# Kernel tuning notes

Measured on AMD Instinct MI355X. Metric: run time of the kernel, lower is better.

## Reference

```python
import jax, jax.numpy as jnp
import numpy as np

D = 64          # dim1 = dim2 = dim3
B = 512         # batch
MMHID = 256
F = (D + 1) ** 3  # 274625, encoder1 input size
SKIP = 3 * (D + 1)  # 195


def _lin(x, w, b):
    # torch nn.Linear: y = x @ W^T + b, W: [out, in]
    return x @ w.T + b


def _bilinear(x1, x2, w, b):
    # torch nn.Bilinear: y_o = x1_i W_{oij} x2_j + b_o
    return jnp.einsum('bi,oij,bj->bo', x1, w, x2) + b


def setup_inputs() -> dict:
    key = jax.random.key(0)
    ks = jax.random.split(key, 16)

    def n(k, shape, scale):
        return (jax.random.normal(k, shape, dtype=jnp.float32) * scale)

    inp = {
        'vec1': n(ks[0], (B, D), 1.0),
        'vec2': n(ks[1], (B, D), 1.0),
        'vec3': n(ks[2], (B, D), 1.0),
        # gated branch 1
        'h1_w': n(ks[3], (D, D), 1.0 / np.sqrt(D)), 'h1_b': jnp.zeros((D,), jnp.float32),
        'z1_w': n(ks[4], (D, D, D), 1.0 / D), 'z1_b': jnp.zeros((D,), jnp.float32),
        'o1_w': n(ks[5], (D, D), 1.0 / np.sqrt(D)), 'o1_b': jnp.zeros((D,), jnp.float32),
        # gated branch 2
        'h2_w': n(ks[6], (D, D), 1.0 / np.sqrt(D)), 'h2_b': jnp.zeros((D,), jnp.float32),
        'z2_w': n(ks[7], (D, D, D), 1.0 / D), 'z2_b': jnp.zeros((D,), jnp.float32),
        'o2_w': n(ks[8], (D, D), 1.0 / np.sqrt(D)), 'o2_b': jnp.zeros((D,), jnp.float32),
        # gated branch 3
        'h3_w': n(ks[9], (D, D), 1.0 / np.sqrt(D)), 'h3_b': jnp.zeros((D,), jnp.float32),
        'z3_w': n(ks[10], (D, D, D), 1.0 / D), 'z3_b': jnp.zeros((D,), jnp.float32),
        'o3_w': n(ks[11], (D, D), 1.0 / np.sqrt(D)), 'o3_b': jnp.zeros((D,), jnp.float32),
        # encoders
        'enc1_w': n(ks[12], (MMHID, F), 1.0 / np.sqrt(F)), 'enc1_b': jnp.zeros((MMHID,), jnp.float32),
        'enc2_w': n(ks[13], (MMHID, MMHID + SKIP), 1.0 / np.sqrt(MMHID + SKIP)), 'enc2_b': jnp.zeros((MMHID,), jnp.float32),
    }
    return inp


def reference(vec1, vec2, vec3,
              h1_w, h1_b, z1_w, z1_b, o1_w, o1_b,
              h2_w, h2_b, z2_w, z2_b, o2_w, o2_b,
              h3_w, h3_b, z3_w, z3_b, o3_w, o3_b,
              enc1_w, enc1_b, enc2_w, enc2_b):
    # dropout layers are identity in eval mode
    h1 = jax.nn.relu(_lin(vec1, h1_w, h1_b))
    z1 = _bilinear(vec1, vec3, z1_w, z1_b)
    o1 = jax.nn.relu(_lin(jax.nn.sigmoid(z1) * h1, o1_w, o1_b))

    h2 = jax.nn.relu(_lin(vec2, h2_w, h2_b))
    z2 = _bilinear(vec2, vec3, z2_w, z2_b)
    o2 = jax.nn.relu(_lin(jax.nn.sigmoid(z2) * h2, o2_w, o2_b))

    h3 = jax.nn.relu(_lin(vec3, h3_w, h3_b))
    z3 = _bilinear(vec1, vec3, z3_w, z3_b)  # note: z3 uses (vec1, vec3) per source
    o3 = jax.nn.relu(_lin(jax.nn.sigmoid(z3) * h3, o3_w, o3_b))

    ones = jnp.ones((o1.shape[0], 1), o1.dtype)
    o1 = jnp.concatenate([o1, ones], axis=1)  # [B, D+1]
    o2 = jnp.concatenate([o2, ones], axis=1)
    o3 = jnp.concatenate([o3, ones], axis=1)

    # trilinear outer product, flattened in (i, j, k) order matching
    # bmm(o1, o2).flatten then bmm(., o3).flatten in torch
    o123 = jnp.einsum('bi,bj,bk->bijk', o1, o2, o3).reshape(o1.shape[0], -1)  # [B, F]

    out = jax.nn.relu(_lin(o123, enc1_w, enc1_b))
    out = jnp.concatenate([out, o1, o2, o3], axis=1)  # skip connection
    out = jax.nn.relu(_lin(out, enc2_w, enc2_b))
    return out
```

## Files before the change

kernel.cpp:

```cpp
#include <hip/hip_runtime.h>
#include <hip/hip_bf16.h>
#include <stdint.h>

typedef unsigned short u16;
typedef unsigned int u32;

#define F1 274625
#define IJ1 4225

typedef float v4f __attribute__((ext_vector_type(4)));
typedef __bf16 v8bf __attribute__((ext_vector_type(8)));

__device__ __forceinline__ float lof(u32 u) { union { u32 u; float f; } c; c.u = u << 16; return c.f; }
__device__ __forceinline__ float hif(u32 u) { union { u32 u; float f; } c; c.u = u & 0xffff0000u; return c.f; }
__device__ __forceinline__ u16 f2bf(float f) {
  union { float f; u32 u; } c; c.f = f;
  u32 r = (c.u >> 16) & 1u;
  return (u16)((c.u + 0x7fffu + r) >> 16);
}
__device__ __forceinline__ u32 pkbf(u32 a, u32 b) {
  union { float f; u32 u; } ca, cb; ca.u = a; cb.u = b;
  __hip_bfloat162 h = __float22bfloat162_rn(make_float2(ca.f, cb.f));
  union { __hip_bfloat162 h; u32 u; } c; c.h = h; return c.u;
}

__global__ void __launch_bounds__(256) k0_transpose(const float* __restrict__ v1,
    const float* __restrict__ v2, const float* __restrict__ v3, float* __restrict__ xT) {
  int g = blockIdx.x * 256 + threadIdx.x;
  if (g >= 3 * 64 * 512) return;
  int t = g >> 15, r = g & 32767;
  int d = r >> 9, b = r & 511;
  const float* v = (t == 0) ? v1 : ((t == 1) ? v2 : v3);
  xT[g] = v[b * 64 + d];
}

__global__ void __launch_bounds__(256) k1_bilinear(
    const float* __restrict__ zw1, const float* __restrict__ zw2, const float* __restrict__ zw3,
    const float* __restrict__ xT, float* __restrict__ zsum) {
  int bid = blockIdx.x;
  int ih = bid & 1, bh = (bid >> 1) & 1;
  int o = (bid >> 2) & 63, t = bid >> 8;
  int b = bh * 256 + threadIdx.x;
  const float* zw = (t == 0) ? zw1 : ((t == 1) ? zw2 : zw3);
  const float* xiT = xT + ((t == 1) ? 32768 : 0);
  const float* x3T = xT + 65536;
  float x3r[64];
#pragma unroll
  for (int j = 0; j < 64; ++j) x3r[j] = x3T[j * 512 + b];
  const float4* w4 = (const float4*)(zw + o * 4096);
  float acc = 0.f;
  int i0 = ih * 32;
#pragma unroll 2
  for (int i = i0; i < i0 + 32; ++i) {
    float xi = xiT[i * 512 + b];
    float s = 0.f;
#pragma unroll
    for (int q = 0; q < 16; ++q) {
      float4 w = w4[i * 16 + q];
      s += w.x * x3r[q*4+0] + w.y * x3r[q*4+1] + w.z * x3r[q*4+2] + w.w * x3r[q*4+3];
    }
    acc += xi * s;
  }
  atomicAdd(&zsum[t * 32768 + o * 512 + b], acc);
}

__global__ void __launch_bounds__(256) k2_branch(
    const float* __restrict__ hw1, const float* __restrict__ hb1,
    const float* __restrict__ ow1, const float* __restrict__ ob1,
    const float* __restrict__ hw2, const float* __restrict__ hb2,
    const float* __restrict__ ow2, const float* __restrict__ ob2,
    const float* __restrict__ hw3, const float* __restrict__ hb3,
    const float* __restrict__ ow3, const float* __restrict__ ob3,
    const float* __restrict__ zb1, const float* __restrict__ zb2, const float* __restrict__ zb3,
    const float* __restrict__ xT, const float* __restrict__ zsum,
    float* __restrict__ oT, u16* __restrict__ o3row) {
  int t = blockIdx.x >> 3, bc = blockIdx.x & 7;
  int lane = threadIdx.x & 63;
  int w = __builtin_amdgcn_readfirstlane((int)(threadIdx.x >> 6));
  int b = bc * 64 + lane;
  const float* hw = (t==0)?hw1:((t==1)?hw2:hw3);
  const float* hb = (t==0)?hb1:((t==1)?hb2:hb3);
  const float* ow = (t==0)?ow1:((t==1)?ow2:ow3);
  const float* ob = (t==0)?ob1:((t==1)?ob2:ob3);
  const float* zb = (t==0)?zb1:((t==1)?zb2:zb3);
  const float* xtT = xT + t * 32768;
  const float4* hw4 = (const float4*)hw;
  const float4* ow4 = (const float4*)ow;
  __shared__ float gT[64][68];
  float xr[64];
#pragma unroll
  for (int k = 0; k < 64; ++k) xr[k] = xtT[k * 512 + b];
#pragma unroll
  for (int ii = 0; ii < 16; ii += 4) {
    float gv[4];
#pragma unroll
    for (int q = 0; q < 4; ++q) {
      int i = w * 16 + ii + q;
      float a = hb[i];
#pragma unroll
      for (int kq = 0; kq < 16; ++kq) {
        float4 h4 = hw4[i * 16 + kq];
        a += h4.x * xr[kq*4+0] + h4.y * xr[kq*4+1] + h4.z * xr[kq*4+2] + h4.w * xr[kq*4+3];
      }
      float hv = fmaxf(a, 0.f);
      float z = zsum[t * 32768 + i * 512 + b] + zb[i];
      float sg = 1.f / (1.f + __expf(-z));
      gv[q] = sg * hv;
    }
    *(float4*)&gT[lane][w * 16 + ii] = make_float4(gv[0], gv[1], gv[2], gv[3]);
  }
  __syncthreads();
  float gr[64];
#pragma unroll
  for (int k = 0; k < 64; k += 4) {
    float4 g4 = *(const float4*)&gT[lane][k];
    gr[k] = g4.x; gr[k+1] = g4.y; gr[k+2] = g4.z; gr[k+3] = g4.w;
  }
#pragma unroll
  for (int ii = 0; ii < 16; ++ii) {
    int oo = w * 16 + ii;
    float a = ob[oo];
#pragma unroll
    for (int kq = 0; kq < 16; ++kq) {
      float4 o4 = ow4[oo * 16 + kq];
      a += o4.x * gr[kq*4+0] + o4.y * gr[kq*4+1] + o4.z * gr[kq*4+2] + o4.w * gr[kq*4+3];
    }
    float ov = fmaxf(a, 0.f);
    oT[(t * 65 + oo) * 512 + b] = ov;
    if (t == 2) o3row[b * 72 + oo] = f2bf(ov);
  }
  if (w == 0) oT[(t * 65 + 64) * 512 + b] = 1.f;
  if (t == 2 && w == 1) {
    uint4 ones = make_uint4(0x3F80u, 0u, 0u, 0u);
    *(uint4*)&o3row[b * 72 + 64] = ones;
  }
}

template<int S4>
__device__ __forceinline__ void pack_row(const uint4* qv, char* bsB, int sxor, int hh) {
  u32 l[36];
#pragma unroll
  for (int r = 0; r < 9; ++r) {
    l[4*r+0] = qv[r].x; l[4*r+1] = qv[r].y; l[4*r+2] = qv[r].z; l[4*r+3] = qv[r].w;
  }
#pragma unroll
  for (int m = 0; m < 4; ++m) {
    u32 p0 = pkbf(l[S4+8*m+0], l[S4+8*m+1]);
    u32 p1 = pkbf(l[S4+8*m+2], l[S4+8*m+3]);
    u32 p2 = pkbf(l[S4+8*m+4], l[S4+8*m+5]);
    u32 p3 = pkbf(l[S4+8*m+6], l[S4+8*m+7]);
    *(uint4*)(bsB + ((hh*64 + m*16) ^ sxor)) = make_uint4(p0, p1, p2, p3);
  }
  if (hh) *(u16*)(bsB + 128) = (u16)(pkbf(l[S4+32], l[S4+32]) & 0xffffu);
}

__global__ void __launch_bounds__(256, 2) k4_gemm(
    const float* __restrict__ W, const u16* __restrict__ o3row,
    const float* __restrict__ oT, float* __restrict__ accum,
    float* __restrict__ pbuf, int mode) {
  __shared__ u16 o3r[128 * 72];
  __shared__ u16 Bs[128 * 72];
  __shared__ float o12sf[128];
  int bid = blockIdx.x;
  int xcd = bid & 7, slot = bid >> 3;
  int mb = slot & 3, ph = slot >> 2;
  int pair = ph * 8 + xcd;
  int sK = pair >> 1, nb = pair & 1;
  int mbase = mb * 128, nbase = nb * 128;
  int ij0 = (sK * IJ1) >> 6, ij1 = ((sK + 1) * IJ1) >> 6;
  int tid = threadIdx.x;

  for (int u = tid; u < 1024; u += 256) {
    int r = u >> 3, c = u & 7;
    const uint4 v = *(const uint4*)(o3row + (mbase + r) * 72 + c * 8);
    *(uint4*)((char*)o3r + r * 144 + ((c * 16) ^ (((r >> 2) & 7) << 4))) = v;
  }

  int lane = tid & 63;
  int wid = __builtin_amdgcn_readfirstlane(tid >> 6);
  int wm = wid >> 1, wn = wid & 1;
  int lrow = lane & 15, lkg = lane >> 4;
  int rpos = lane >> 1, hh = lane & 1;

  int aoffB[4][2], boffB[4][2], vvoff[4];
#pragma unroll
  for (int u = 0; u < 4; ++u) {
    int ra = wm * 64 + u * 16 + lrow;
    int rb = wn * 64 + u * 16 + lrow;
#pragma unroll
    for (int k2 = 0; k2 < 2; ++k2) {
      aoffB[u][k2] = ra * 144 + ((lkg * 16 + k2 * 64) ^ (((ra >> 2) & 7) << 4));
      boffB[u][k2] = rb * 144 + ((lkg * 16 + k2 * 64) ^ (((rb >> 2) & 7) << 4));
    }
    vvoff[u] = rb * 72 + 64;
  }

  v4f acc[16] = {};
  const uint4* Wq = (const uint4*)W;
  uint4 qv[9];
  float cA = 0.f, cB = 0.f;
  {
    int cc = (wid - ij0) & 3;
    int row = rpos * 4 + cc;
    long g = (long)(nbase + row) * F1 + (long)ij0 * 65;
    long u4 = (g >> 2) + (long)hh * 8;
#pragma unroll
    for (int r = 0; r < 9; ++r) qv[r] = Wq[u4 + r];
    int i = ij0 / 65, j = ij0 - i * 65;
    if (tid < 128) {
      cA = oT[i * 512 + mbase + tid];
      cB = oT[(65 + j) * 512 + mbase + tid];
    }
  }
  __syncthreads();

#pragma unroll 1
  for (int ij = ij0; ij < ij1; ++ij) {
    {
      int cc = (wid - ij) & 3;
      int row = rpos * 4 + cc;
      char* bsB = (char*)Bs + row * 144;
      int sxor = ((row >> 2) & 7) << 4;
      if      (wid == 0) pack_row<0>(qv, bsB, sxor, hh);
      else if (wid == 1) pack_row<1>(qv, bsB, sxor, hh);
      else if (wid == 2) pack_row<2>(qv, bsB, sxor, hh);
      else               pack_row<3>(qv, bsB, sxor, hh);
    }
    if (tid < 128) o12sf[tid] = cA * cB;
    if (ij + 1 < ij1) {
      int cc = (wid - (ij + 1)) & 3;
      int row = rpos * 4 + cc;
      long g = (long)(nbase + row) * F1 + (long)(ij + 1) * 65;
      long u4 = (g >> 2) + (long)hh * 8;
#pragma unroll
      for (int r = 0; r < 9; ++r) qv[r] = Wq[u4 + r];
      int i = (ij + 1) / 65, j = (ij + 1) - i * 65;
      if (tid < 128) {
        cA = oT[i * 512 + mbase + tid];
        cB = oT[(65 + j) * 512 + mbase + tid];
      }
    }
    __syncthreads();

    v8bf bf0[2], bf1[2], bf2[2], bf3[2];
#pragma unroll
    for (int k2 = 0; k2 < 2; ++k2) {
      bf0[k2] = *(const v8bf*)((const char*)Bs + boffB[0][k2]);
      bf1[k2] = *(const v8bf*)((const char*)Bs + boffB[1][k2]);
      bf2[k2] = *(const v8bf*)((const char*)Bs + boffB[2][k2]);
      bf3[k2] = *(const v8bf*)((const char*)Bs + boffB[3][k2]);
    }
    float vv0 = lof((u32)Bs[vvoff[0]]);
    float vv1 = lof((u32)Bs[vvoff[1]]);
    float vv2 = lof((u32)Bs[vvoff[2]]);
    float vv3 = lof((u32)Bs[vvoff[3]]);
#pragma unroll
    for (int t2 = 0; t2 < 4; ++t2) {
      v8bf a0 = *(const v8bf*)((const char*)o3r + aoffB[t2][0]);
      v8bf a1 = *(const v8bf*)((const char*)o3r + aoffB[t2][1]);
      v4f P0 = {}, P1 = {}, P2 = {}, P3 = {};
      P0 = __builtin_amdgcn_mfma_f32_16x16x32_bf16(a0, bf0[0], P0, 0, 0, 0);
      P0 = __builtin_amdgcn_mfma_f32_16x16x32_bf16(a1, bf0[1], P0, 0, 0, 0);
      P1 = __builtin_amdgcn_mfma_f32_16x16x32_bf16(a0, bf1[0], P1, 0, 0, 0);
      P1 = __builtin_amdgcn_mfma_f32_16x16x32_bf16(a1, bf1[1], P1, 0, 0, 0);
      P2 = __builtin_amdgcn_mfma_f32_16x16x32_bf16(a0, bf2[0], P2, 0, 0, 0);
      P2 = __builtin_amdgcn_mfma_f32_16x16x32_bf16(a1, bf2[1], P2, 0, 0, 0);
      P3 = __builtin_amdgcn_mfma_f32_16x16x32_bf16(a0, bf3[0], P3, 0, 0, 0);
      P3 = __builtin_amdgcn_mfma_f32_16x16x32_bf16(a1, bf3[1], P3, 0, 0, 0);
      float4 sp = *(const float4*)&o12sf[wm * 64 + t2 * 16 + lkg * 4];
#pragma unroll
      for (int e = 0; e < 4; ++e) {
        float se = (e == 0) ? sp.x : (e == 1) ? sp.y : (e == 2) ? sp.z : sp.w;
        acc[t2 * 4 + 0][e] += se * (P0[e] + vv0);
        acc[t2 * 4 + 1][e] += se * (P1[e] + vv1);
        acc[t2 * 4 + 2][e] += se * (P2[e] + vv2);
        acc[t2 * 4 + 3][e] += se * (P3[e] + vv3);
      }
    }
    __syncthreads();
  }

  if (mode) {
    float* dst = pbuf + ((long)sK << 17);
#pragma unroll
    for (int t2 = 0; t2 < 4; ++t2) {
      int gb0 = mbase + wm * 64 + t2 * 16 + lkg * 4;
#pragma unroll
      for (int u2 = 0; u2 < 4; ++u2) {
        int go = nbase + wn * 64 + u2 * 16 + lrow;
#pragma unroll
        for (int e = 0; e < 4; ++e)
          dst[(gb0 + e) * 256 + go] = acc[t2 * 4 + u2][e];
      }
    }
  } else {
#pragma unroll
    for (int t2 = 0; t2 < 4; ++t2) {
      int gb0 = mbase + wm * 64 + t2 * 16 + lkg * 4;
#pragma unroll
      for (int u2 = 0; u2 < 4; ++u2) {
        int go = nbase + wn * 64 + u2 * 16 + lrow;
#pragma unroll
        for (int e = 0; e < 4; ++e)
          atomicAdd(&accum[(gb0 + e) * 256 + go], acc[t2 * 4 + u2][e]);
      }
    }
  }
}

__global__ void __launch_bounds__(256) k4_reduce(const float* __restrict__ P,
                                                 float* __restrict__ accum) {
  int g = blockIdx.x * 256 + threadIdx.x;
  const v4f* p4 = (const v4f*)P;
  v4f s = p4[g];
#pragma unroll 4
  for (int k = 1; k < 64; ++k) s += p4[(k << 15) + g];
  ((v4f*)accum)[g] = s;
}

__global__ void __launch_bounds__(256) k5_enc2(
    const float* __restrict__ accum, const float* __restrict__ oT,
    const float* __restrict__ enc1b, const float* __restrict__ w2,
    const float* __restrict__ enc2b, float* __restrict__ outp) {
  int bg = blockIdx.x >> 3, og = blockIdx.x & 7;
  int lane = threadIdx.x & 63;
  int w = __builtin_amdgcn_readfirstlane((int)(threadIdx.x >> 6));
  int b = bg * 64 + lane;
  int obase = og * 32 + w * 8;
  float a8[8];
#pragma unroll
  for (int q = 0; q < 8; ++q) a8[q] = enc2b[obase + q];
  for (int c = 0; c < 256; ++c) {
    float x = fmaxf(accum[b * 256 + c] + enc1b[c], 0.f);
#pragma unroll
    for (int q = 0; q < 8; ++q) a8[q] += w2[(obase + q) * 451 + c] * x;
  }
  for (int e = 0; e < 195; ++e) {
    float x = oT[e * 512 + b];
#pragma unroll
    for (int q = 0; q < 8; ++q) a8[q] += w2[(obase + q) * 451 + 256 + e] * x;
  }
#pragma unroll
  for (int q = 0; q < 8; ++q) outp[b * 256 + obase + q] = fmaxf(a8[q], 0.f);
}

extern "C" void kernel_launch(void* const* d_in, const int* in_sizes, int n_in,
                              void* d_out, int out_size, void* d_ws, size_t ws_size,
                              hipStream_t stream) {
  const float* vec1 = (const float*)d_in[0];
  const float* vec2 = (const float*)d_in[1];
  const float* vec3 = (const float*)d_in[2];
  const float* h1w = (const float*)d_in[3];  const float* h1b = (const float*)d_in[4];
  const float* z1w = (const float*)d_in[5];  const float* z1b = (const float*)d_in[6];
  const float* o1w = (const float*)d_in[7];  const float* o1b = (const float*)d_in[8];
  const float* h2w = (const float*)d_in[9];  const float* h2b = (const float*)d_in[10];
  const float* z2w = (const float*)d_in[11]; const float* z2b = (const float*)d_in[12];
  const float* o2w = (const float*)d_in[13]; const float* o2b = (const float*)d_in[14];
  const float* h3w = (const float*)d_in[15]; const float* h3b = (const float*)d_in[16];
  const float* z3w = (const float*)d_in[17]; const float* z3b = (const float*)d_in[18];
  const float* o3w = (const float*)d_in[19]; const float* o3b = (const float*)d_in[20];
  const float* e1w = (const float*)d_in[21]; const float* e1b = (const float*)d_in[22];
  const float* e2w = (const float*)d_in[23]; const float* e2b = (const float*)d_in[24];

  char* ws = (char*)d_ws;
  float* accum = (float*)(ws + 0);
  float* oT    = (float*)(ws + 524288);
  u16* o3row   = (u16*)  (ws + 923648);
  float* xT    = (float*)(ws + 997376);
  float* zsum  = (float*)(ws + 1390592);
  float* pbuf  = (float*)(ws + 1783808);
  size_t need = 1783808 + (size_t)64 * 512 * 256 * 4;
  int mode = (ws_size >= need) ? 1 : 0;
  float* pArg = mode ? pbuf : accum;

  hipMemsetAsync(accum, 0, 524288, stream);
  hipMemsetAsync(zsum, 0, 393216, stream);

  hipLaunchKernelGGL(k0_transpose, dim3(384), dim3(256), 0, stream, vec1, vec2, vec3, xT);
  hipLaunchKernelGGL(k1_bilinear, dim3(768), dim3(256), 0, stream, z1w, z2w, z3w, xT, zsum);
  hipLaunchKernelGGL(k2_branch, dim3(24), dim3(256), 0, stream,
                     h1w, h1b, o1w, o1b, h2w, h2b, o2w, o2b, h3w, h3b, o3w, o3b,
                     z1b, z2b, z3b, xT, zsum, oT, o3row);
  hipLaunchKernelGGL(k4_gemm, dim3(512), dim3(256), 0, stream, e1w, o3row, oT, accum,
                     pArg, mode);
  if (mode)
    hipLaunchKernelGGL(k4_reduce, dim3(128), dim3(256), 0, stream, pbuf, accum);
  hipLaunchKernelGGL(k5_enc2, dim3(64), dim3(256), 0, stream, accum, oT, e1b, e2w, e2b,
                     (float*)d_out);
}
```

Measured before the change: 720.7 us.

## Double-buffer enc1 GEMM tiles, shrink M tile, drop transpose and memsets

The enc1 GEMM now uses 64-row M tiles with 1024 blocks and three blocks per CU. It double-buffers the packed bf16 weight tile in shared memory, so packing the next ij step overlaps with the MFMAs, and it raises wave priority around the MFMA section. The separate transpose kernel is removed: the bilinear and branch kernels read vec rows directly with float4 loads. The bilinear kernel covers the full i range per block and writes directly instead of using atomics, so the memsets are dropped. The reduce kernel now applies bias and ReLU and writes a transposed layout for enc2. The cost is that the XOR swizzle is removed from shared memory, which can bring back bank conflicts, and each weight tile is reused across a smaller M tile.

```diff
diff --git a/kernel.cpp b/kernel.cpp
--- a/kernel.cpp
+++ b/kernel.cpp
@@ -12,7 +12,6 @@
 typedef __bf16 v8bf __attribute__((ext_vector_type(8)));
 
 __device__ __forceinline__ float lof(u32 u) { union { u32 u; float f; } c; c.u = u << 16; return c.f; }
-__device__ __forceinline__ float hif(u32 u) { union { u32 u; float f; } c; c.u = u & 0xffff0000u; return c.f; }
 __device__ __forceinline__ u16 f2bf(float f) {
   union { float f; u32 u; } c; c.f = f;
   u32 r = (c.u >> 16) & 1u;
@@ -24,35 +23,28 @@
   union { __hip_bfloat162 h; u32 u; } c; c.h = h; return c.u;
 }
 
-__global__ void __launch_bounds__(256) k0_transpose(const float* __restrict__ v1,
-    const float* __restrict__ v2, const float* __restrict__ v3, float* __restrict__ xT) {
-  int g = blockIdx.x * 256 + threadIdx.x;
-  if (g >= 3 * 64 * 512) return;
-  int t = g >> 15, r = g & 32767;
-  int d = r >> 9, b = r & 511;
-  const float* v = (t == 0) ? v1 : ((t == 1) ? v2 : v3);
-  xT[g] = v[b * 64 + d];
-}
-
 __global__ void __launch_bounds__(256) k1_bilinear(
+    const float* __restrict__ v1, const float* __restrict__ v2, const float* __restrict__ v3,
     const float* __restrict__ zw1, const float* __restrict__ zw2, const float* __restrict__ zw3,
-    const float* __restrict__ xT, float* __restrict__ zsum) {
+    float* __restrict__ zsum) {
   int bid = blockIdx.x;
-  int ih = bid & 1, bh = (bid >> 1) & 1;
-  int o = (bid >> 2) & 63, t = bid >> 8;
+  int bh = bid & 1, o = (bid >> 1) & 63, t = bid >> 7;
   int b = bh * 256 + threadIdx.x;
   const float* zw = (t == 0) ? zw1 : ((t == 1) ? zw2 : zw3);
-  const float* xiT = xT + ((t == 1) ? 32768 : 0);
-  const float* x3T = xT + 65536;
+  const float* xv = (t == 1) ? v2 : v1;
   float x3r[64];
-#pragma unroll
-  for (int j = 0; j < 64; ++j) x3r[j] = x3T[j * 512 + b];
+  const float4* x34 = (const float4*)(v3 + b * 64);
+#pragma unroll
+  for (int q = 0; q < 16; ++q) {
+    float4 a = x34[q];
+    x3r[q*4+0] = a.x; x3r[q*4+1] = a.y; x3r[q*4+2] = a.z; x3r[q*4+3] = a.w;
+  }
   const float4* w4 = (const float4*)(zw + o * 4096);
+  const float* xrow = xv + b * 64;
   float acc = 0.f;
-  int i0 = ih * 32;
-#pragma unroll 2
-  for (int i = i0; i < i0 + 32; ++i) {
-    float xi = xiT[i * 512 + b];
+#pragma unroll 4
+  for (int i = 0; i < 64; ++i) {
+    float xi = xrow[i];
     float s = 0.f;
 #pragma unroll
     for (int q = 0; q < 16; ++q) {
@@ -61,10 +53,11 @@
     }
     acc += xi * s;
   }
-  atomicAdd(&zsum[t * 32768 + o * 512 + b], acc);
+  zsum[t * 32768 + o * 512 + b] = acc;
 }
 
 __global__ void __launch_bounds__(256) k2_branch(
+    const float* __restrict__ v1, const float* __restrict__ v2, const float* __restrict__ v3,
     const float* __restrict__ hw1, const float* __restrict__ hb1,
     const float* __restrict__ ow1, const float* __restrict__ ob1,
     const float* __restrict__ hw2, const float* __restrict__ hb2,
@@ -72,7 +65,7 @@
     const float* __restrict__ hw3, const float* __restrict__ hb3,
     const float* __restrict__ ow3, const float* __restrict__ ob3,
     const float* __restrict__ zb1, const float* __restrict__ zb2, const float* __restrict__ zb3,
-    const float* __restrict__ xT, const float* __restrict__ zsum,
+    const float* __restrict__ zsum,
     float* __restrict__ oT, u16* __restrict__ o3row) {
   int t = blockIdx.x >> 3, bc = blockIdx.x & 7;
   int lane = threadIdx.x & 63;
@@ -83,13 +76,17 @@
   const float* ow = (t==0)?ow1:((t==1)?ow2:ow3);
   const float* ob = (t==0)?ob1:((t==1)?ob2:ob3);
   const float* zb = (t==0)?zb1:((t==1)?zb2:zb3);
-  const float* xtT = xT + t * 32768;
+  const float* xv = (t==0)?v1:((t==1)?v2:v3);
   const float4* hw4 = (const float4*)hw;
   const float4* ow4 = (const float4*)ow;
   __shared__ float gT[64][68];
   float xr[64];
-#pragma unroll
-  for (int k = 0; k < 64; ++k) xr[k] = xtT[k * 512 + b];
+  const float4* xv4 = (const float4*)(xv + b * 64);
+#pragma unroll
+  for (int q = 0; q < 16; ++q) {
+    float4 a = xv4[q];
+    xr[q*4+0] = a.x; xr[q*4+1] = a.y; xr[q*4+2] = a.z; xr[q*4+3] = a.w;
+  }
 #pragma unroll
   for (int ii = 0; ii < 16; ii += 4) {
     float gv[4];
@@ -137,7 +134,7 @@
 }
 
 template<int S4>
-__device__ __forceinline__ void pack_row(const uint4* qv, char* bsB, int sxor, int hh) {
+__device__ __forceinline__ void pack_row(const uint4* qv, u16* bp, int hh) {
   u32 l[36];
 #pragma unroll
   for (int r = 0; r < 9; ++r) {
@@ -149,179 +146,154 @@
     u32 p1 = pkbf(l[S4+8*m+2], l[S4+8*m+3]);
     u32 p2 = pkbf(l[S4+8*m+4], l[S4+8*m+5]);
     u32 p3 = pkbf(l[S4+8*m+6], l[S4+8*m+7]);
-    *(uint4*)(bsB + ((hh*64 + m*16) ^ sxor)) = make_uint4(p0, p1, p2, p3);
-  }
-  if (hh) *(u16*)(bsB + 128) = (u16)(pkbf(l[S4+32], l[S4+32]) & 0xffffu);
-}
-
-__global__ void __launch_bounds__(256, 2) k4_gemm(
+    *(uint4*)(bp + hh * 32 + m * 8) = make_uint4(p0, p1, p2, p3);
+  }
+  if (hh) bp[64] = (u16)(pkbf(l[S4+32], l[S4+32]) & 0xffffu);
+}
+
+__global__ void __launch_bounds__(256, 3) k4_gemm(
     const float* __restrict__ W, const u16* __restrict__ o3row,
     const float* __restrict__ oT, float* __restrict__ accum,
     float* __restrict__ pbuf, int mode) {
-  __shared__ u16 o3r[128 * 72];
-  __shared__ u16 Bs[128 * 72];
-  __shared__ float o12sf[128];
+  __shared__ u16 o3r[64 * 72];
+  __shared__ u16 Bs[2][128 * 72];
+  __shared__ float o12sf[2][64];
   int bid = blockIdx.x;
   int xcd = bid & 7, slot = bid >> 3;
-  int mb = slot & 3, ph = slot >> 2;
+  int mb = slot & 7, ph = slot >> 3;
   int pair = ph * 8 + xcd;
   int sK = pair >> 1, nb = pair & 1;
-  int mbase = mb * 128, nbase = nb * 128;
+  int mbase = mb * 64, nbase = nb * 128;
   int ij0 = (sK * IJ1) >> 6, ij1 = ((sK + 1) * IJ1) >> 6;
   int tid = threadIdx.x;
-
-  for (int u = tid; u < 1024; u += 256) {
-    int r = u >> 3, c = u & 7;
-    const uint4 v = *(const uint4*)(o3row + (mbase + r) * 72 + c * 8);
-    *(uint4*)((char*)o3r + r * 144 + ((c * 16) ^ (((r >> 2) & 7) << 4))) = v;
-  }
-
+  {
+    const uint4* src = (const uint4*)(o3row + mbase * 72);
+    uint4* dst = (uint4*)o3r;
+    for (int u = tid; u < 576; u += 256) dst[u] = src[u];
+  }
   int lane = tid & 63;
   int wid = __builtin_amdgcn_readfirstlane(tid >> 6);
-  int wm = wid >> 1, wn = wid & 1;
   int lrow = lane & 15, lkg = lane >> 4;
   int rpos = lane >> 1, hh = lane & 1;
 
-  int aoffB[4][2], boffB[4][2], vvoff[4];
-#pragma unroll
-  for (int u = 0; u < 4; ++u) {
-    int ra = wm * 64 + u * 16 + lrow;
-    int rb = wn * 64 + u * 16 + lrow;
-#pragma unroll
-    for (int k2 = 0; k2 < 2; ++k2) {
-      aoffB[u][k2] = ra * 144 + ((lkg * 16 + k2 * 64) ^ (((ra >> 2) & 7) << 4));
-      boffB[u][k2] = rb * 144 + ((lkg * 16 + k2 * 64) ^ (((rb >> 2) & 7) << 4));
-    }
-    vvoff[u] = rb * 72 + 64;
-  }
-
-  v4f acc[16] = {};
+  v4f acc[8] = {};
   const uint4* Wq = (const uint4*)W;
   uint4 qv[9];
   float cA = 0.f, cB = 0.f;
-  {
-    int cc = (wid - ij0) & 3;
+
+  auto loadW = [&](int ij) {
+    int cc = (wid - ij) & 3;
     int row = rpos * 4 + cc;
-    long g = (long)(nbase + row) * F1 + (long)ij0 * 65;
+    long g = (long)(nbase + row) * F1 + (long)ij * 65;
     long u4 = (g >> 2) + (long)hh * 8;
 #pragma unroll
     for (int r = 0; r < 9; ++r) qv[r] = Wq[u4 + r];
-    int i = ij0 / 65, j = ij0 - i * 65;
-    if (tid < 128) {
+  };
+  auto loadO = [&](int ij) {
+    if (tid < 64) {
+      int i = ij / 65, j = ij - i * 65;
       cA = oT[i * 512 + mbase + tid];
       cB = oT[(65 + j) * 512 + mbase + tid];
     }
-  }
+  };
+  auto packCur = [&](int ij, int buf) {
+    int cc = (wid - ij) & 3;
+    int row = rpos * 4 + cc;
+    u16* bp = &Bs[buf][row * 72];
+    if      (wid == 0) pack_row<0>(qv, bp, hh);
+    else if (wid == 1) pack_row<1>(qv, bp, hh);
+    else if (wid == 2) pack_row<2>(qv, bp, hh);
+    else               pack_row<3>(qv, bp, hh);
+    if (tid < 64) o12sf[buf][tid] = cA * cB;
+  };
+
+  loadW(ij0); loadO(ij0);
   __syncthreads();
+  packCur(ij0, 0);
+  loadW(ij0 + 1); loadO(ij0 + 1);
+  asm volatile("s_waitcnt lgkmcnt(0)\n\ts_barrier" ::: "memory");
 
 #pragma unroll 1
   for (int ij = ij0; ij < ij1; ++ij) {
-    {
-      int cc = (wid - ij) & 3;
-      int row = rpos * 4 + cc;
-      char* bsB = (char*)Bs + row * 144;
-      int sxor = ((row >> 2) & 7) << 4;
-      if      (wid == 0) pack_row<0>(qv, bsB, sxor, hh);
-      else if (wid == 1) pack_row<1>(qv, bsB, sxor, hh);
-      else if (wid == 2) pack_row<2>(qv, bsB, sxor, hh);
-      else               pack_row<3>(qv, bsB, sxor, hh);
-    }
-    if (tid < 128) o12sf[tid] = cA * cB;
+    int cur = (ij - ij0) & 1;
     if (ij + 1 < ij1) {
-      int cc = (wid - (ij + 1)) & 3;
-      int row = rpos * 4 + cc;
-      long g = (long)(nbase + row) * F1 + (long)(ij + 1) * 65;
-      long u4 = (g >> 2) + (long)hh * 8;
-#pragma unroll
-      for (int r = 0; r < 9; ++r) qv[r] = Wq[u4 + r];
-      int i = (ij + 1) / 65, j = (ij + 1) - i * 65;
-      if (tid < 128) {
-        cA = oT[i * 512 + mbase + tid];
-        cB = oT[(65 + j) * 512 + mbase + tid];
-      }
-    }
-    __syncthreads();
-
-    v8bf bf0[2], bf1[2], bf2[2], bf3[2];
-#pragma unroll
-    for (int k2 = 0; k2 < 2; ++k2) {
-      bf0[k2] = *(const v8bf*)((const char*)Bs + boffB[0][k2]);
-      bf1[k2] = *(const v8bf*)((const char*)Bs + boffB[1][k2]);
-      bf2[k2] = *(const v8bf*)((const char*)Bs + boffB[2][k2]);
-      bf3[k2] = *(const v8bf*)((const char*)Bs + boffB[3][k2]);
-    }
-    float vv0 = lof((u32)Bs[vvoff[0]]);
-    float vv1 = lof((u32)Bs[vvoff[1]]);
-    float vv2 = lof((u32)Bs[vvoff[2]]);
-    float vv3 = lof((u32)Bs[vvoff[3]]);
+      packCur(ij + 1, cur ^ 1);
+      if (ij + 2 < ij1) { loadW(ij + 2); loadO(ij + 2); }
+    }
+    const u16* bs = Bs[cur];
+    v8bf bf00 = *(const v8bf*)&bs[(wid * 32 +  0 + lrow) * 72 + lkg * 8];
+    v8bf bf01 = *(const v8bf*)&bs[(wid * 32 +  0 + lrow) * 72 + lkg * 8 + 32];
+    v8bf bf10 = *(const v8bf*)&bs[(wid * 32 + 16 + lrow) * 72 + lkg * 8];
+    v8bf bf11 = *(const v8bf*)&bs[(wid * 32 + 16 + lrow) * 72 + lkg * 8 + 32];
+    float vv0 = lof((u32)bs[(wid * 32 +  0 + lrow) * 72 + 64]);
+    float vv1 = lof((u32)bs[(wid * 32 + 16 + lrow) * 72 + 64]);
+    __builtin_amdgcn_s_setprio(1);
 #pragma unroll
     for (int t2 = 0; t2 < 4; ++t2) {
-      v8bf a0 = *(const v8bf*)((const char*)o3r + aoffB[t2][0]);
-      v8bf a1 = *(const v8bf*)((const char*)o3r + aoffB[t2][1]);
-      v4f P0 = {}, P1 = {}, P2 = {}, P3 = {};
-      P0 = __builtin_amdgcn_mfma_f32_16x16x32_bf16(a0, bf0[0], P0, 0, 0, 0);
-      P0 = __builtin_amdgcn_mfma_f32_16x16x32_bf16(a1, bf0[1], P0, 0, 0, 0);
-      P1 = __builtin_amdgcn_mfma_f32_16x16x32_bf16(a0, bf1[0], P1, 0, 0, 0);
-      P1 = __builtin_amdgcn_mfma_f32_16x16x32_bf16(a1, bf1[1], P1, 0, 0, 0);
-      P2 = __builtin_amdgcn_mfma_f32_16x16x32_bf16(a0, bf2[0], P2, 0, 0, 0);
-      P2 = __builtin_amdgcn_mfma_f32_16x16x32_bf16(a1, bf2[1], P2, 0, 0, 0);
-      P3 = __builtin_amdgcn_mfma_f32_16x16x32_bf16(a0, bf3[0], P3, 0, 0, 0);
-      P3 = __builtin_amdgcn_mfma_f32_16x16x32_bf16(a1, bf3[1], P3, 0, 0, 0);
-      float4 sp = *(const float4*)&o12sf[wm * 64 + t2 * 16 + lkg * 4];
+      v8bf a0 = *(const v8bf*)&o3r[(t2 * 16 + lrow) * 72 + lkg * 8];
+      v8bf a1 = *(const v8bf*)&o3r[(t2 * 16 + lrow) * 72 + lkg * 8 + 32];
+      v4f P0 = {}, P1 = {};
+      P0 = __builtin_amdgcn_mfma_f32_16x16x32_bf16(a0, bf00, P0, 0, 0, 0);
+      P0 = __builtin_amdgcn_mfma_f32_16x16x32_bf16(a1, bf01, P0, 0, 0, 0);
+      P1 = __builtin_amdgcn_mfma_f32_16x16x32_bf16(a0, bf10, P1, 0, 0, 0);
+      P1 = __builtin_amdgcn_mfma_f32_16x16x32_bf16(a1, bf11, P1, 0, 0, 0);
+      float4 sp = *(const float4*)&o12sf[cur][t2 * 16 + lkg * 4];
 #pragma unroll
       for (int e = 0; e < 4; ++e) {
         float se = (e == 0) ? sp.x : (e == 1) ? sp.y : (e == 2) ? sp.z : sp.w;
-        acc[t2 * 4 + 0][e] += se * (P0[e] + vv0);
-        acc[t2 * 4 + 1][e] += se * (P1[e] + vv1);
-        acc[t2 * 4 + 2][e] += se * (P2[e] + vv2);
-        acc[t2 * 4 + 3][e] += se * (P3[e] + vv3);
+        acc[t2 * 2 + 0][e] += se * (P0[e] + vv0);
+        acc[t2 * 2 + 1][e] += se * (P1[e] + vv1);
       }
     }
-    __syncthreads();
+    __builtin_amdgcn_s_setprio(0);
+    asm volatile("s_waitcnt lgkmcnt(0)\n\ts_barrier" ::: "memory");
   }
 
   if (mode) {
     float* dst = pbuf + ((long)sK << 17);
 #pragma unroll
     for (int t2 = 0; t2 < 4; ++t2) {
-      int gb0 = mbase + wm * 64 + t2 * 16 + lkg * 4;
-#pragma unroll
-      for (int u2 = 0; u2 < 4; ++u2) {
-        int go = nbase + wn * 64 + u2 * 16 + lrow;
+      int gb0 = mbase + t2 * 16 + lkg * 4;
+#pragma unroll
+      for (int u2 = 0; u2 < 2; ++u2) {
+        int go = nbase + wid * 32 + u2 * 16 + lrow;
 #pragma unroll
         for (int e = 0; e < 4; ++e)
-          dst[(gb0 + e) * 256 + go] = acc[t2 * 4 + u2][e];
+          dst[(gb0 + e) * 256 + go] = acc[t2 * 2 + u2][e];
       }
     }
   } else {
 #pragma unroll
     for (int t2 = 0; t2 < 4; ++t2) {
-      int gb0 = mbase + wm * 64 + t2 * 16 + lkg * 4;
-#pragma unroll
-      for (int u2 = 0; u2 < 4; ++u2) {
-        int go = nbase + wn * 64 + u2 * 16 + lrow;
+      int gb0 = mbase + t2 * 16 + lkg * 4;
+#pragma unroll
+      for (int u2 = 0; u2 < 2; ++u2) {
+        int go = nbase + wid * 32 + u2 * 16 + lrow;
 #pragma unroll
         for (int e = 0; e < 4; ++e)
-          atomicAdd(&accum[(gb0 + e) * 256 + go], acc[t2 * 4 + u2][e]);
+          atomicAdd(&accum[(gb0 + e) * 256 + go], acc[t2 * 2 + u2][e]);
       }
     }
   }
 }
 
 __global__ void __launch_bounds__(256) k4_reduce(const float* __restrict__ P,
-                                                 float* __restrict__ accum) {
+    const float* __restrict__ e1b, float* __restrict__ xrT) {
   int g = blockIdx.x * 256 + threadIdx.x;
   const v4f* p4 = (const v4f*)P;
   v4f s = p4[g];
 #pragma unroll 4
   for (int k = 1; k < 64; ++k) s += p4[(k << 15) + g];
-  ((v4f*)accum)[g] = s;
+  int b = g >> 6, c0 = (g & 63) << 2;
+#pragma unroll
+  for (int e = 0; e < 4; ++e)
+    xrT[(c0 + e) * 512 + b] = fmaxf(s[e] + e1b[c0 + e], 0.f);
 }
 
 __global__ void __launch_bounds__(256) k5_enc2(
-    const float* __restrict__ accum, const float* __restrict__ oT,
+    const float* __restrict__ xin, const float* __restrict__ oT,
     const float* __restrict__ enc1b, const float* __restrict__ w2,
-    const float* __restrict__ enc2b, float* __restrict__ outp) {
+    const float* __restrict__ enc2b, float* __restrict__ outp, int mode) {
   int bg = blockIdx.x >> 3, og = blockIdx.x & 7;
   int lane = threadIdx.x & 63;
   int w = __builtin_amdgcn_readfirstlane((int)(threadIdx.x >> 6));
@@ -330,10 +302,18 @@
   float a8[8];
 #pragma unroll
   for (int q = 0; q < 8; ++q) a8[q] = enc2b[obase + q];
-  for (int c = 0; c < 256; ++c) {
-    float x = fmaxf(accum[b * 256 + c] + enc1b[c], 0.f);
-#pragma unroll
-    for (int q = 0; q < 8; ++q) a8[q] += w2[(obase + q) * 451 + c] * x;
+  if (mode) {
+    for (int c = 0; c < 256; ++c) {
+      float x = xin[c * 512 + b];
+#pragma unroll
+      for (int q = 0; q < 8; ++q) a8[q] += w2[(obase + q) * 451 + c] * x;
+    }
+  } else {
+    for (int c = 0; c < 256; ++c) {
+      float x = fmaxf(xin[b * 256 + c] + enc1b[c], 0.f);
+#pragma unroll
+      for (int q = 0; q < 8; ++q) a8[q] += w2[(obase + q) * 451 + c] * x;
+    }
   }
   for (int e = 0; e < 195; ++e) {
     float x = oT[e * 512 + b];
@@ -366,25 +346,24 @@
   float* accum = (float*)(ws + 0);
   float* oT    = (float*)(ws + 524288);
   u16* o3row   = (u16*)  (ws + 923648);
-  float* xT    = (float*)(ws + 997376);
-  float* zsum  = (float*)(ws + 1390592);
-  float* pbuf  = (float*)(ws + 1783808);
-  size_t need = 1783808 + (size_t)64 * 512 * 256 * 4;
+  float* zsum  = (float*)(ws + 997376);
+  float* pbuf  = (float*)(ws + 1390592);
+  size_t need = 1390592 + (size_t)64 * 512 * 256 * 4;
   int mode = (ws_size >= need) ? 1 : 0;
   float* pArg = mode ? pbuf : accum;
 
-  hipMemsetAsync(accum, 0, 524288, stream);
-  hipMemsetAsync(zsum, 0, 393216, stream);
-
-  hipLaunchKernelGGL(k0_transpose, dim3(384), dim3(256), 0, stream, vec1, vec2, vec3, xT);
-  hipLaunchKernelGGL(k1_bilinear, dim3(768), dim3(256), 0, stream, z1w, z2w, z3w, xT, zsum);
+  if (!mode) hipMemsetAsync(accum, 0, 524288, stream);
+
+  hipLaunchKernelGGL(k1_bilinear, dim3(384), dim3(256), 0, stream,
+                     vec1, vec2, vec3, z1w, z2w, z3w, zsum);
   hipLaunchKernelGGL(k2_branch, dim3(24), dim3(256), 0, stream,
+                     vec1, vec2, vec3,
                      h1w, h1b, o1w, o1b, h2w, h2b, o2w, o2b, h3w, h3b, o3w, o3b,
-                     z1b, z2b, z3b, xT, zsum, oT, o3row);
-  hipLaunchKernelGGL(k4_gemm, dim3(512), dim3(256), 0, stream, e1w, o3row, oT, accum,
+                     z1b, z2b, z3b, zsum, oT, o3row);
+  hipLaunchKernelGGL(k4_gemm, dim3(1024), dim3(256), 0, stream, e1w, o3row, oT, accum,
                      pArg, mode);
   if (mode)
-    hipLaunchKernelGGL(k4_reduce, dim3(128), dim3(256), 0, stream, pbuf, accum);
+    hipLaunchKernelGGL(k4_reduce, dim3(128), dim3(256), 0, stream, pbuf, e1b, accum);
   hipLaunchKernelGGL(k5_enc2, dim3(64), dim3(256), 0, stream, accum, oT, e1b, e2w, e2b,
-                     (float*)d_out);
-}
+                     (float*)d_out, mode);
+}
```

After: 902.6 us. 1.25x slower.
